# Kernel optimization log

Hardware: AMD Instinct MI355X
Metric: run time of the kernel (lower is better)

## Reference

```python
import jax, jax.numpy as jnp
import numpy as np

THRESH = 0.7
N_MIN = 16 * 512 * 512 // 16  # 262144
IGNORE_LB = 1


def setup_inputs() -> dict:
    key = jax.random.key(0)
    k1, k2 = jax.random.split(key)
    logits = jax.random.normal(k1, (16, 19, 512, 512), dtype=jnp.float32)
    labels = jax.random.randint(k2, (16, 512, 512), 0, 19)
    return {"logits": logits, "labels": labels}


def reference(logits, labels):
    # Per-pixel cross-entropy with ignore_index semantics (loss=0 at ignored pixels)
    logp = jax.nn.log_softmax(logits, axis=1)                     # [N,C,H,W]
    picked = jnp.take_along_axis(logp, labels[:, None], axis=1)  # [N,1,H,W]
    loss = -picked[:, 0].reshape(-1)                              # [N*H*W]
    valid = labels.reshape(-1) != IGNORE_LB
    loss = jnp.where(valid, loss, 0.0)

    thresh = -jnp.log(jnp.asarray(THRESH, dtype=loss.dtype))

    # Top-n_min valid losses (descending); invalid pixels pushed to -inf.
    masked = jnp.where(valid, loss, -jnp.inf)
    top, _ = jax.lax.top_k(masked, N_MIN)
    kth = top[N_MIN - 1]

    # Branch 1: mean of all valid losses > thresh
    keep_gt = valid & (loss > thresh)
    cnt_gt = jnp.sum(keep_gt)
    mean_gt = jnp.sum(jnp.where(keep_gt, loss, 0.0)) / jnp.maximum(cnt_gt, 1).astype(loss.dtype)
    # Branch 2: mean of top n_min losses
    mean_top = jnp.mean(top)

    return jnp.where(kth > thresh, mean_gt, mean_top)
```

## Files before the change

kernel.cpp:

```cpp
#include <hip/hip_runtime.h>
#include <math.h>

#define NPIX  4194304
#define HW    262144
#define NCH   19
#define KSEL  262144u
#define IGN   1
#define THRESH_F 0.35667494393873245f

#define P1BLK 4096
#define HBLK  256
#define HTHR  65536

__device__ void select_from_hist(const unsigned int* __restrict__ gh, int nbins,
                                 unsigned int need, int* res)
{
    __shared__ unsigned int sh[2048];
    __shared__ unsigned int ssum[256];
    const int tid = threadIdx.x;
    for (int i = tid; i < nbins; i += 256) sh[i] = gh[i];
    __syncthreads();
    const int per = nbins >> 8;
    const int base = tid * per;
    unsigned int p = 0;
    for (int i = 0; i < per; ++i) p += sh[base + i];
    ssum[tid] = p;
    __syncthreads();
    for (int off = 1; off < 256; off <<= 1) {
        unsigned int add = (tid + off < 256) ? ssum[tid + off] : 0u;
        __syncthreads();
        ssum[tid] += add;
        __syncthreads();
    }
    unsigned int Sme   = ssum[tid];
    unsigned int Snext = (tid < 255) ? ssum[tid + 1] : 0u;
    if (Sme >= need && Snext < need) {
        unsigned int above = Snext;
        int bin = base;
        for (int b = base + per - 1; b >= base; --b) {
            unsigned int c = sh[b];
            if (above + c >= need) { bin = b; break; }
            above += c;
        }
        res[0] = bin; res[1] = (int)above;
    }
    if (tid == 0 && ssum[0] < need) { res[0] = 0; res[1] = 0; }
    __syncthreads();
}

__global__ __launch_bounds__(256) void k_loss(
    const float* __restrict__ logits, const int* __restrict__ labels,
    float* __restrict__ losses,
    float* __restrict__ psum, unsigned int* __restrict__ pcnt)
{
    const int p0 = (blockIdx.x * 256 + threadIdx.x) * 4;
    const int n  = p0 >> 18;
    const int hw = p0 & (HW - 1);
    const float* base = logits + (size_t)n * (NCH * HW) + hw;

    float4 vals[NCH];
    #pragma unroll
    for (int c = 0; c < NCH; ++c)
        vals[c] = *(const float4*)(base + (size_t)c * HW);
    const int4 lab4 = *(const int4*)(labels + p0);
    const int labs[4] = {lab4.x, lab4.y, lab4.z, lab4.w};

    float lsum = 0.f;
    unsigned int lcnt = 0u;
    float out4[4];

    #pragma unroll
    for (int j = 0; j < 4; ++j) {
        float m = -__builtin_inff(), picked = 0.f;
        #pragma unroll
        for (int c = 0; c < NCH; ++c) {
            float x = (j == 0) ? vals[c].x : (j == 1) ? vals[c].y : (j == 2) ? vals[c].z : vals[c].w;
            m = fmaxf(m, x);
            if (c == labs[j]) picked = x;
        }
        float s = 0.f;
        #pragma unroll
        for (int c = 0; c < NCH; ++c) {
            float x = (j == 0) ? vals[c].x : (j == 1) ? vals[c].y : (j == 2) ? vals[c].z : vals[c].w;
            s += __expf(x - m);
        }
        float loss = m + logf(s) - picked;
        bool valid = (labs[j] != IGN);
        out4[j] = valid ? loss : -__builtin_inff();
        if (valid & (loss > THRESH_F)) { lsum += loss; lcnt++; }
    }
    *(float4*)(losses + p0) = make_float4(out4[0], out4[1], out4[2], out4[3]);

    #pragma unroll
    for (int o = 32; o > 0; o >>= 1) { lsum += __shfl_down(lsum, o); lcnt += __shfl_down(lcnt, o); }
    __shared__ float  s_sum[4];
    __shared__ unsigned int s_cnt[4];
    int wid = threadIdx.x >> 6;
    if ((threadIdx.x & 63) == 0) { s_sum[wid] = lsum; s_cnt[wid] = lcnt; }
    __syncthreads();
    if (threadIdx.x == 0) {
        psum[blockIdx.x] = s_sum[0] + s_sum[1] + s_sum[2] + s_sum[3];
        pcnt[blockIdx.x] = s_cnt[0] + s_cnt[1] + s_cnt[2] + s_cnt[3];
    }
}

__global__ __launch_bounds__(256) void k_hist1(
    const float* __restrict__ losses, unsigned int* __restrict__ hist1)
{
    __shared__ unsigned int lh[2048];
    for (int i = threadIdx.x; i < 2048; i += 256) lh[i] = 0u;
    __syncthreads();

    const uint4* l4 = (const uint4*)losses;
    for (int i = blockIdx.x * 256 + threadIdx.x; i < NPIX / 4; i += HTHR) {
        uint4 w4 = l4[i];
        const unsigned int wv[4] = {w4.x, w4.y, w4.z, w4.w};
        #pragma unroll
        for (int j = 0; j < 4; ++j) {
            unsigned int w = wv[j];
            if (!(w & 0x80000000u)) atomicAdd(&lh[w >> 21], 1u);
        }
    }
    __syncthreads();
    for (int i = threadIdx.x; i < 2048; i += 256) {
        unsigned int c = lh[i];
        if (c) atomicAdd(&hist1[i], c);
    }
}

__global__ __launch_bounds__(256) void k_hist2(
    const float* __restrict__ losses, const unsigned int* __restrict__ hist1,
    unsigned int* __restrict__ hist2, double* __restrict__ ghi1)
{
    __shared__ int res[2];
    select_from_hist(hist1, 2048, KSEL, res);
    const int B1 = res[0];

    __shared__ unsigned int lh[2048];
    for (int i = threadIdx.x; i < 2048; i += 256) lh[i] = 0u;
    __syncthreads();

    const uint4* l4 = (const uint4*)losses;
    float lsum = 0.f;
    for (int i = blockIdx.x * 256 + threadIdx.x; i < NPIX / 4; i += HTHR) {
        uint4 w4 = l4[i];
        const unsigned int wv[4] = {w4.x, w4.y, w4.z, w4.w};
        #pragma unroll
        for (int j = 0; j < 4; ++j) {
            unsigned int w = wv[j];
            if (w & 0x80000000u) continue;
            int b1 = (int)(w >> 21);
            if (b1 == B1)      atomicAdd(&lh[(w >> 10) & 0x7FFu], 1u);
            else if (b1 > B1)  lsum += __uint_as_float(w);
        }
    }
    __syncthreads();
    for (int i = threadIdx.x; i < 2048; i += 256)
        if (lh[i]) atomicAdd(&hist2[i], lh[i]);

    #pragma unroll
    for (int o = 32; o > 0; o >>= 1) lsum += __shfl_down(lsum, o);
    __shared__ float wsum[4];
    int wid = threadIdx.x >> 6;
    if ((threadIdx.x & 63) == 0) wsum[wid] = lsum;
    __syncthreads();
    if (threadIdx.x == 0)
        ghi1[blockIdx.x] = (double)(wsum[0] + wsum[1] + wsum[2] + wsum[3]);
}

__global__ __launch_bounds__(256) void k_hist3(
    const float* __restrict__ losses, const unsigned int* __restrict__ hist1,
    const unsigned int* __restrict__ hist2, unsigned int* __restrict__ hist3,
    double* __restrict__ ghi2)
{
    __shared__ int res[2];
    select_from_hist(hist1, 2048, KSEL, res);
    const int B1 = res[0];
    const unsigned int a1 = (unsigned int)res[1];
    select_from_hist(hist2, 2048, KSEL - a1, res);
    const int B2 = res[0];

    __shared__ unsigned int lh[1024];
    for (int i = threadIdx.x; i < 1024; i += 256) lh[i] = 0u;
    __syncthreads();

    const uint4* l4 = (const uint4*)losses;
    float lsum = 0.f;
    for (int i = blockIdx.x * 256 + threadIdx.x; i < NPIX / 4; i += HTHR) {
        uint4 w4 = l4[i];
        const unsigned int wv[4] = {w4.x, w4.y, w4.z, w4.w};
        #pragma unroll
        for (int j = 0; j < 4; ++j) {
            unsigned int w = wv[j];
            if (w & 0x80000000u) continue;
            if ((int)(w >> 21) != B1) continue;
            int b2 = (int)((w >> 10) & 0x7FFu);
            if (b2 == B2)      atomicAdd(&lh[w & 0x3FFu], 1u);
            else if (b2 > B2)  lsum += __uint_as_float(w);
        }
    }
    __syncthreads();
    for (int i = threadIdx.x; i < 1024; i += 256)
        if (lh[i]) atomicAdd(&hist3[i], lh[i]);

    #pragma unroll
    for (int o = 32; o > 0; o >>= 1) lsum += __shfl_down(lsum, o);
    __shared__ float wsum[4];
    int wid = threadIdx.x >> 6;
    if ((threadIdx.x & 63) == 0) wsum[wid] = lsum;
    __syncthreads();
    if (threadIdx.x == 0)
        ghi2[blockIdx.x] = (double)(wsum[0] + wsum[1] + wsum[2] + wsum[3]);
}

__global__ __launch_bounds__(256) void k_final(
    const unsigned int* __restrict__ hist1, const unsigned int* __restrict__ hist2,
    const unsigned int* __restrict__ hist3,
    const float* __restrict__ psum, const unsigned int* __restrict__ pcnt,
    const double* __restrict__ ghi1, const double* __restrict__ ghi2,
    float* __restrict__ out)
{
    const int tid = threadIdx.x;

    double my_sum = 0.0;
    unsigned long long my_cnt = 0ull;
    #pragma unroll
    for (int i = 0; i < 16; ++i) {
        my_sum += (double)psum[tid * 16 + i];
        my_cnt += (unsigned long long)pcnt[tid * 16 + i];
    }
    double my_hi = ghi1[tid] + ghi2[tid] - ghi2[tid];
    double my_hi2 = ghi2[tid];
    #pragma unroll
    for (int o = 32; o > 0; o >>= 1) {
        my_sum += __shfl_down(my_sum, o);
        my_cnt += __shfl_down(my_cnt, o);
        my_hi  += __shfl_down(my_hi, o);
        my_hi2 += __shfl_down(my_hi2, o);
    }
    __shared__ double r_sumw[4], r_hiw[4], r_hi2w[4];
    __shared__ unsigned long long r_cntw[4];
    int wid = tid >> 6;
    if ((tid & 63) == 0) { r_sumw[wid] = my_sum; r_cntw[wid] = my_cnt; r_hiw[wid] = my_hi; r_hi2w[wid] = my_hi2; }
    __syncthreads();
    __shared__ double t_sum_gt, t_hi1, t_hi2;
    __shared__ unsigned long long t_cnt_gt;
    if (tid == 0) {
        t_sum_gt = r_sumw[0] + r_sumw[1] + r_sumw[2] + r_sumw[3];
        t_cnt_gt = r_cntw[0] + r_cntw[1] + r_cntw[2] + r_cntw[3];
        t_hi1    = r_hiw[0] + r_hiw[1] + r_hiw[2] + r_hiw[3];
        t_hi2    = r_hi2w[0] + r_hi2w[1] + r_hi2w[2] + r_hi2w[3];
    }
    __syncthreads();

    __shared__ int res[2];
    select_from_hist(hist1, 2048, KSEL, res);
    const int B1 = res[0];
    const unsigned int a1 = (unsigned int)res[1];
    select_from_hist(hist2, 2048, KSEL - a1, res);
    const int B2 = res[0];
    const unsigned int a2 = (unsigned int)res[1];
    const unsigned int need3 = KSEL - a1 - a2;
    const unsigned int hibits = ((unsigned int)B1 << 21) | ((unsigned int)B2 << 10);

    __shared__ unsigned int h3[1024];
    __shared__ unsigned int c_suf[256];
    __shared__ double s_suf[256];
    for (int i = tid; i < 1024; i += 256) h3[i] = hist3[i];
    __syncthreads();
    unsigned int cp = 0; double sp = 0.0;
    #pragma unroll
    for (int i = 0; i < 4; ++i) {
        int b = tid * 4 + i;
        unsigned int c = h3[b];
        cp += c;
        sp += (double)c * (double)__uint_as_float(hibits | (unsigned int)b);
    }
    c_suf[tid] = cp; s_suf[tid] = sp;
    __syncthreads();
    for (int off = 1; off < 256; off <<= 1) {
        unsigned int ca = (tid + off < 256) ? c_suf[tid + off] : 0u;
        double sa = (tid + off < 256) ? s_suf[tid + off] : 0.0;
        __syncthreads();
        c_suf[tid] += ca; s_suf[tid] += sa;
        __syncthreads();
    }
    __shared__ int r_l;
    __shared__ unsigned int r_above;
    __shared__ double r_sum3;
    unsigned int Sme   = c_suf[tid];
    unsigned int Snext = (tid < 255) ? c_suf[tid + 1] : 0u;
    double       Wnext = (tid < 255) ? s_suf[tid + 1] : 0.0;
    if (Sme >= need3 && Snext < need3) {
        unsigned int above = Snext;
        double sum3 = Wnext;
        int l = tid * 4;
        for (int b = tid * 4 + 3; b >= tid * 4; --b) {
            unsigned int c = h3[b];
            if (above + c >= need3) { l = b; break; }
            above += c;
            sum3 += (double)c * (double)__uint_as_float(hibits | (unsigned int)b);
        }
        r_l = l; r_above = above; r_sum3 = sum3;
    }
    if (tid == 0 && c_suf[0] < need3) { r_l = 0; r_above = 0; r_sum3 = 0.0; }
    __syncthreads();

    if (tid == 0) {
        float v = __uint_as_float(hibits | (unsigned int)r_l);
        unsigned long long cnt_above = (unsigned long long)a1 + a2 + r_above;
        double sum_above = t_hi1 + t_hi2 + r_sum3;
        double mean_top = (sum_above + (double)(KSEL - cnt_above) * (double)v) / (double)KSEL;
        double result;
        if (v > THRESH_F) {
            unsigned long long cg = t_cnt_gt;
            result = t_sum_gt / (double)(cg > 0ull ? cg : 1ull);
        } else {
            result = mean_top;
        }
        out[0] = (float)result;
    }
}

extern "C" void kernel_launch(void* const* d_in, const int* in_sizes, int n_in,
                              void* d_out, int out_size, void* d_ws, size_t ws_size,
                              hipStream_t stream)
{
    const float* logits = (const float*)d_in[0];
    const int*   labels = (const int*)d_in[1];
    float* out = (float*)d_out;

    unsigned int* hist1 = (unsigned int*)d_ws;
    unsigned int* hist2 = hist1 + 2048;
    unsigned int* hist3 = hist2 + 2048;
    float*        psum  = (float*)((char*)d_ws + 20480);
    unsigned int* pcnt  = (unsigned int*)((char*)d_ws + 36864);
    double*       ghi1  = (double*)((char*)d_ws + 53248);
    double*       ghi2  = (double*)((char*)d_ws + 55296);
    float*        losses = (float*)((char*)d_ws + 65536);

    hipMemsetAsync(d_ws, 0, 20480, stream);

    k_loss <<<dim3(P1BLK), dim3(256), 0, stream>>>(logits, labels, losses, psum, pcnt);
    k_hist1<<<dim3(HBLK),  dim3(256), 0, stream>>>(losses, hist1);
    k_hist2<<<dim3(HBLK),  dim3(256), 0, stream>>>(losses, hist1, hist2, ghi1);
    k_hist3<<<dim3(HBLK),  dim3(256), 0, stream>>>(losses, hist1, hist2, hist3, ghi2);
    k_final<<<dim3(1),     dim3(256), 0, stream>>>(hist1, hist2, hist3, psum, pcnt, ghi1, ghi2, out);
}
```

Before: 472.6 us.

## Stream logits in channel groups with online softmax to cut register pressure

The loss kernel no longer loads all 19 channel float4s up front. It processes channels in groups of 5 and keeps a running max and rescaled sum per pixel (online log-sum-exp), which lowers VGPR usage and allows launch_bounds to request 6 waves. Loads now use nontemporal hints and logf becomes __logf, which trades a little accuracy and extra exp rescaling for higher occupancy. A redundant add and subtract in the final kernel is also removed.

```diff
diff --git a/kernel.cpp b/kernel.cpp
--- a/kernel.cpp
+++ b/kernel.cpp
@@ -11,6 +11,8 @@
 #define P1BLK 4096
 #define HBLK  256
 #define HTHR  65536
+
+typedef float vfloat4 __attribute__((ext_vector_type(4)));
 
 __device__ void select_from_hist(const unsigned int* __restrict__ gh, int nbins,
                                  unsigned int need, int* res)
@@ -48,7 +50,7 @@
     __syncthreads();
 }
 
-__global__ __launch_bounds__(256) void k_loss(
+__global__ __launch_bounds__(256, 6) void k_loss(
     const float* __restrict__ logits, const int* __restrict__ labels,
     float* __restrict__ losses,
     float* __restrict__ psum, unsigned int* __restrict__ pcnt)
@@ -58,33 +60,44 @@
     const int hw = p0 & (HW - 1);
     const float* base = logits + (size_t)n * (NCH * HW) + hw;
 
-    float4 vals[NCH];
-    #pragma unroll
-    for (int c = 0; c < NCH; ++c)
-        vals[c] = *(const float4*)(base + (size_t)c * HW);
     const int4 lab4 = *(const int4*)(labels + p0);
     const int labs[4] = {lab4.x, lab4.y, lab4.z, lab4.w};
+
+    float m[4], s[4], pk[4];
+    #pragma unroll
+    for (int j = 0; j < 4; ++j) { m[j] = -__builtin_inff(); s[j] = 0.f; pk[j] = 0.f; }
+
+    int c = 0;
+    #pragma unroll
+    for (int g = 0; g < 4; ++g) {
+        const int sz = (g < 3) ? 5 : 4;
+        vfloat4 x[5];
+        #pragma unroll
+        for (int i = 0; i < 5; ++i)
+            if (i < sz)
+                x[i] = __builtin_nontemporal_load((const vfloat4*)(base + (size_t)(c + i) * HW));
+        #pragma unroll
+        for (int j = 0; j < 4; ++j) {
+            float gm = x[0][j];
+            #pragma unroll
+            for (int i = 1; i < 5; ++i) if (i < sz) gm = fmaxf(gm, x[i][j]);
+            float mn  = fmaxf(m[j], gm);
+            float acc = s[j] * __expf(m[j] - mn);
+            #pragma unroll
+            for (int i = 0; i < 5; ++i) if (i < sz) acc += __expf(x[i][j] - mn);
+            s[j] = acc; m[j] = mn;
+            #pragma unroll
+            for (int i = 0; i < 5; ++i) if (i < sz) pk[j] += (c + i == labs[j]) ? x[i][j] : 0.f;
+        }
+        c += sz;
+    }
 
     float lsum = 0.f;
     unsigned int lcnt = 0u;
     float out4[4];
-
     #pragma unroll
     for (int j = 0; j < 4; ++j) {
-        float m = -__builtin_inff(), picked = 0.f;
-        #pragma unroll
-        for (int c = 0; c < NCH; ++c) {
-            float x = (j == 0) ? vals[c].x : (j == 1) ? vals[c].y : (j == 2) ? vals[c].z : vals[c].w;
-            m = fmaxf(m, x);
-            if (c == labs[j]) picked = x;
-        }
-        float s = 0.f;
-        #pragma unroll
-        for (int c = 0; c < NCH; ++c) {
-            float x = (j == 0) ? vals[c].x : (j == 1) ? vals[c].y : (j == 2) ? vals[c].z : vals[c].w;
-            s += __expf(x - m);
-        }
-        float loss = m + logf(s) - picked;
+        float loss = m[j] + __logf(s[j]) - pk[j];
         bool valid = (labs[j] != IGN);
         out4[j] = valid ? loss : -__builtin_inff();
         if (valid & (loss > THRESH_F)) { lsum += loss; lcnt++; }
@@ -229,7 +242,7 @@
         my_sum += (double)psum[tid * 16 + i];
         my_cnt += (unsigned long long)pcnt[tid * 16 + i];
     }
-    double my_hi = ghi1[tid] + ghi2[tid] - ghi2[tid];
+    double my_hi  = ghi1[tid];
     double my_hi2 = ghi2[tid];
     #pragma unroll
     for (int o = 32; o > 0; o >>= 1) {
```

After: 472.9 us. About the same (+0.1%).
